# Kernel optimization log

Hardware: AMD Instinct MI355X
Metric: run time of the kernel (lower is better)

The kernel has to match this reference:

```python
import jax, jax.numpy as jnp
import numpy as np

DIM = 1024
HEADS = 16
DIM_HEAD = DIM // HEADS
SCALE = DIM_HEAD ** -0.5


def setup_inputs() -> dict:
    key = jax.random.key(0)
    k1, k2, k3 = jax.random.split(key, 3)
    x = jax.random.normal(k1, (4, 2048, DIM), dtype=jnp.float32)
    # q_lin: Linear(dim, 3*dim, bias=False); store as [dim, 3*dim] for x @ W
    w_qkv = jax.random.normal(k2, (DIM, 3 * DIM), dtype=jnp.float32) * (DIM ** -0.5)
    w_out = jax.random.normal(k3, (DIM, DIM), dtype=jnp.float32) * (DIM ** -0.5)
    return {"x": x, "w_qkv": w_qkv, "w_out": w_out}


def reference(x, w_qkv, w_out):
    b, n, d = x.shape
    qkv = x @ w_qkv  # [b, n, 3d]
    q, k, v = jnp.split(qkv, 3, axis=-1)
    # b n (h d) -> b h n d
    def to_heads(t):
        return t.reshape(b, n, HEADS, DIM_HEAD).transpose(0, 2, 1, 3)
    q, k, v = to_heads(q), to_heads(k), to_heads(v)
    sim = jnp.einsum('bhnj,bhmj->bhnm', q, k) * SCALE
    causal = jnp.triu(jnp.ones((n, n), dtype=bool), k=1)
    sim = jnp.where(causal, -jnp.finfo(sim.dtype).max, sim)
    attn = jax.nn.softmax(sim, axis=-1)
    out = jnp.einsum('bhnm,bhmd->bhnd', attn, v)
    out = out.transpose(0, 2, 1, 3).reshape(b, n, d)  # b h n d -> b n (h d)
    return out @ w_out
```

## Files before the change

kernel.cpp:

```cpp
#include <hip/hip_runtime.h>
#include <hip/hip_bf16.h>
#include <stdint.h>

#define SEQ  2048
#define DIMM 1024
#define NH   16
#define DH   64
#define NB   4
#define MROWS (NB*SEQ)
#define QKP  2080

typedef __attribute__((ext_vector_type(8))) short bf16x8;
typedef __attribute__((ext_vector_type(4))) float f32x4;
typedef __attribute__((ext_vector_type(16))) float f32x16;

#define LOG2E 1.44269504088896340736f

__device__ __forceinline__ unsigned short f2bf(float f) {
    union { float f; uint32_t u; } c; c.f = f;
    uint32_t r = c.u + 0x7fff + ((c.u >> 16) & 1);
    return (unsigned short)(r >> 16);
}

__device__ __forceinline__ void gload_lds16(const void* g, void* lds) {
    __builtin_amdgcn_global_load_lds(
        (const __attribute__((address_space(1))) unsigned int*)(g),
        (__attribute__((address_space(3))) unsigned int*)(lds),
        16, 0, 0);
}

__global__ __launch_bounds__(256) void k_prep(const float* __restrict__ x,
                                              unsigned short* __restrict__ x_bf,
                                              const float* __restrict__ w_qkv,
                                              unsigned short* __restrict__ wqkvT,
                                              const float* __restrict__ w_out,
                                              unsigned short* __restrict__ woutT) {
    __shared__ unsigned short tile[32][33];
    const int bid = blockIdx.x;
    if (bid < 8192) {
        int i = bid * 256 + threadIdx.x;
        float4 v = ((const float4*)x)[i];
        ushort4 o;
        o.x = f2bf(v.x); o.y = f2bf(v.y); o.z = f2bf(v.z); o.w = f2bf(v.w);
        ((ushort4*)x_bf)[i] = o;
        return;
    }
    const float* W;
    unsigned short* Wt;
    int tn, tk, N;
    if (bid < 8192 + 3072) {
        W = w_qkv; Wt = wqkvT; N = 3072;
        tn = (bid - 8192) % 96; tk = (bid - 8192) / 96;
    } else {
        W = w_out; Wt = woutT; N = 1024;
        tn = (bid - 11264) % 32; tk = (bid - 11264) / 32;
    }
    const int K = 1024;
    int lx = threadIdx.x & 31, ly = threadIdx.x >> 5;
    #pragma unroll
    for (int i = 0; i < 32; i += 8) {
        int k = tk * 32 + ly + i;
        int n = tn * 32 + lx;
        tile[ly + i][lx] = f2bf(W[(size_t)k * N + n]);
    }
    __syncthreads();
    int k2 = tk * 32 + lx;
    #pragma unroll
    for (int i = 0; i < 32; i += 8) {
        int n2 = tn * 32 + ly + i;
        Wt[(size_t)n2 * K + k2] = tile[lx][ly + i];
    }
}

template<int MODE>
__global__ __launch_bounds__(256) void k_gemm_bt(const unsigned short* __restrict__ A,
                                                 const unsigned short* __restrict__ Bt,
                                                 void* __restrict__ Cv,
                                                 unsigned short* __restrict__ vtv,
                                                 int M, int N_, int K) {
    constexpr int BM = 128, BN = 128, BK = 64;
    __shared__ unsigned short lA[BM * BK];
    __shared__ unsigned short lB[BN * BK];
    const int ntile = N_ / BN;
    const int tm = blockIdx.x / ntile;
    const int tn = blockIdx.x % ntile;
    const int t = threadIdx.x;
    const int w = t >> 6, l = t & 63;
    const int wr = w >> 1, wc = w & 1;

    const unsigned short* Abase = A + (size_t)tm * BM * K;
    const unsigned short* Bbase = Bt + (size_t)tn * BN * K;

    f32x4 acc[4][4] = {};

    const int rswz = (l & 7) << 4;

    for (int k0 = 0; k0 < K; k0 += BK) {
        __syncthreads();
        #pragma unroll
        for (int i = 0; i < 4; ++i) {
            const int o  = i * 4096 + t * 16;
            const int so = o ^ (((o >> 7) & 7) << 4);
            const int row = so >> 7;
            const int kb  = so & 127;
            gload_lds16((const char*)(Abase + (size_t)row * K + k0) + kb,
                        (char*)lA + i * 4096 + w * 1024);
            gload_lds16((const char*)(Bbase + (size_t)row * K + k0) + kb,
                        (char*)lB + i * 4096 + w * 1024);
        }
        __syncthreads();

        #pragma unroll
        for (int kk = 0; kk < 2; ++kk) {
            bf16x8 af[4], bfv[4];
            #pragma unroll
            for (int i = 0; i < 4; ++i) {
                const int ea = ((wr * 64 + i * 16 + (l & 15)) << 7) + kk * 64 + ((l >> 4) << 4);
                af[i] = *(const bf16x8*)((const char*)lA + (ea ^ rswz));
            }
            #pragma unroll
            for (int j = 0; j < 4; ++j) {
                const int eb = ((wc * 64 + j * 16 + (l & 15)) << 7) + kk * 64 + ((l >> 4) << 4);
                bfv[j] = *(const bf16x8*)((const char*)lB + (eb ^ rswz));
            }
            #pragma unroll
            for (int i = 0; i < 4; ++i)
                #pragma unroll
                for (int j = 0; j < 4; ++j)
                    acc[i][j] = __builtin_amdgcn_mfma_f32_16x16x32_bf16(af[i], bfv[j], acc[i][j], 0, 0, 0);
        }
    }

    const int row0 = tm * BM + wr * 64 + (l >> 4) * 4;
    const int col0 = tn * BN + wc * 64 + (l & 15);

    if (MODE == 0) {
        float* Cf = (float*)Cv;
        #pragma unroll
        for (int i = 0; i < 4; ++i)
            #pragma unroll
            for (int j = 0; j < 4; ++j)
                #pragma unroll
                for (int r = 0; r < 4; ++r)
                    Cf[(size_t)(row0 + i * 16 + r) * N_ + (col0 + j * 16)] = acc[i][j][r];
    } else if (tn < 16) {
        const float cs = (tn < 8) ? 0.125f * LOG2E : 1.0f;
        unsigned short* qk = (unsigned short*)Cv;
        #pragma unroll
        for (int i = 0; i < 4; ++i)
            #pragma unroll
            for (int j = 0; j < 4; ++j)
                #pragma unroll
                for (int r = 0; r < 4; ++r)
                    qk[(size_t)(row0 + i * 16 + r) * QKP + (col0 + j * 16)] = f2bf(acc[i][j][r] * cs);
    } else {
        #pragma unroll
        for (int i = 0; i < 4; ++i) {
            const int rbase = row0 + i * 16;
            const int bq = rbase >> 11;
            const int n0 = rbase & 2047;
            #pragma unroll
            for (int j = 0; j < 4; ++j) {
                const int c = col0 + j * 16 - 2048;
                const int hh = c >> 6, dd = c & 63;
                uint2 u;
                u.x = (unsigned int)f2bf(acc[i][j][0]) | ((unsigned int)f2bf(acc[i][j][1]) << 16);
                u.y = (unsigned int)f2bf(acc[i][j][2]) | ((unsigned int)f2bf(acc[i][j][3]) << 16);
                *(uint2*)(vtv + ((size_t)(bq * 16 + hh) * 64 + dd) * QKP + n0) = u;
            }
        }
    }
}

__global__ __launch_bounds__(256, 2) void k_attn16(const unsigned short* __restrict__ qk,
                                                   const unsigned short* __restrict__ vt,
                                                   unsigned short* __restrict__ out) {
    const int wid = (blockIdx.x & 7) * 64 + (blockIdx.x >> 3);
    const int bh = wid >> 3;
    const int pair = wid & 7;
    const int b = bh >> 4, h = bh & 15;
    const int w = threadIdx.x >> 6, l = threadIdx.x & 63;
    const int l31 = l & 31, hi = l >> 5;

    const unsigned short* qp = qk + (size_t)(b * SEQ) * QKP + h * 64;
    unsigned short* op = out + (size_t)(b * SEQ) * DIMM + h * 64;

    constexpr int KSTEP = 64 * QKP * 2;
    constexpr int VSTEP = 64 * 2;

    union U8 { uint32_t u[4]; bf16x8 v; };

    for (int ci = 0; ci < 2; ++ci) {
        const int chunk = ci ? pair : 15 - pair;
        const int q0w = chunk * 128 + w * 32;
        const int qrow = q0w + l31;
        const int nt = (q0w >> 6) + 1;

        bf16x8 qf[4];
        #pragma unroll
        for (int m = 0; m < 4; ++m)
            qf[m] = *(const bf16x8*)(qp + (size_t)(q0w + l31) * QKP + m * 16 + hi * 8);

        f32x16 accO0 = {}, accO1 = {};
        float m_run = -INFINITY, l_run = 0.f;

        const char* kp0 = (const char*)(qk + ((size_t)b * SEQ + l31) * QKP + 1024 + h * 64 + hi * 8);
        const char* kp1 = kp0 + 32 * QKP * 2;
        const char* vp0 = (const char*)(vt + ((size_t)bh * 64 + l31) * QKP + hi * 8);
        const char* vp1 = vp0 + 32 * QKP * 2;

        bf16x8 kf[2][4];
        #pragma unroll
        for (int m = 0; m < 4; ++m) {
            kf[0][m] = *(const bf16x8*)(kp0 + m * 32);
            kf[1][m] = *(const bf16x8*)(kp1 + m * 32);
        }
        kp0 += KSTEP; kp1 += KSTEP;

        for (int kt = 0; kt < nt; ++kt) {
            const int kv0 = kt * 64;
            const bool msk = (kt == nt - 1);

            f32x16 s0 = {}, s1 = {};
            __builtin_amdgcn_s_setprio(1);
            #pragma unroll
            for (int m = 0; m < 4; ++m) {
                s0 = __builtin_amdgcn_mfma_f32_32x32x16_bf16(kf[0][m], qf[m], s0, 0, 0, 0);
                s1 = __builtin_amdgcn_mfma_f32_32x32x16_bf16(kf[1][m], qf[m], s1, 0, 0, 0);
            }
            __builtin_amdgcn_s_setprio(0);

            bf16x8 vf0[4], vf1[4];
            #pragma unroll
            for (int m = 0; m < 4; ++m) {
                vf0[m] = *(const bf16x8*)(vp0 + m * 32);
                vf1[m] = *(const bf16x8*)(vp1 + m * 32);
            }
            vp0 += VSTEP; vp1 += VSTEP;

            #pragma unroll
            for (int m = 0; m < 4; ++m) {
                kf[0][m] = *(const bf16x8*)(kp0 + m * 32);
                kf[1][m] = *(const bf16x8*)(kp1 + m * 32);
            }
            kp0 += KSTEP; kp1 += KSTEP;

            float tmax = -1e30f;
            #pragma unroll
            for (int r = 0; r < 16; ++r) {
                const int crow = (r & 3) + 8 * (r >> 2) + 4 * hi;
                float v0 = s0[r];
                float v1 = s1[r];
                if (msk) {
                    if (kv0 + crow > qrow)      v0 = -1e30f;
                    if (kv0 + 32 + crow > qrow) v1 = -1e30f;
                }
                s0[r] = v0; s1[r] = v1;
                tmax = fmaxf(tmax, fmaxf(v0, v1));
            }
            tmax = fmaxf(tmax, __shfl_xor(tmax, 32));
            const bool defer = __all(tmax <= m_run + 8.0f);
            float fct = 1.0f;
            if (!defer) {
                const float mnew = fmaxf(m_run, tmax);
                fct = exp2f(m_run - mnew);
                m_run = mnew;
                #pragma unroll
                for (int r = 0; r < 16; ++r) { accO0[r] *= fct; accO1[r] *= fct; }
            }
            float ps = 0.f;
            #pragma unroll
            for (int r = 0; r < 16; ++r) {
                float p0 = exp2f(s0[r] - m_run);
                float p1 = exp2f(s1[r] - m_run);
                s0[r] = p0; s1[r] = p1;
                ps += p0 + p1;
            }
            ps += __shfl_xor(ps, 32);
            l_run = l_run * fct + ps;

            uint32_t pw0[8], pw1[8];
            #pragma unroll
            for (int i = 0; i < 8; ++i) {
                asm("v_cvt_pk_bf16_f32 %0, %1, %2" : "=v"(pw0[i]) : "v"(s0[2*i]), "v"(s0[2*i+1]));
                asm("v_cvt_pk_bf16_f32 %0, %1, %2" : "=v"(pw1[i]) : "v"(s1[2*i]), "v"(s1[2*i+1]));
            }
            __builtin_amdgcn_s_setprio(1);
            #define PVCHUNK(PW, BASE, VF0, VF1) do {                                     \
                uint32_t a0 = PW[BASE+0], b0 = PW[BASE+2];                               \
                uint32_t a1 = PW[BASE+1], b1 = PW[BASE+3];                               \
                asm("v_permlane32_swap_b32 %0, %1" : "+v"(a0), "+v"(b0));                \
                asm("v_permlane32_swap_b32 %0, %1" : "+v"(a1), "+v"(b1));                \
                U8 pb; pb.u[0] = a0; pb.u[1] = a1; pb.u[2] = b0; pb.u[3] = b1;           \
                accO0 = __builtin_amdgcn_mfma_f32_32x32x16_bf16(VF0, pb.v, accO0, 0, 0, 0); \
                accO1 = __builtin_amdgcn_mfma_f32_32x32x16_bf16(VF1, pb.v, accO1, 0, 0, 0); \
            } while (0)
            PVCHUNK(pw0, 0, vf0[0], vf1[0]);
            PVCHUNK(pw0, 4, vf0[1], vf1[1]);
            PVCHUNK(pw1, 0, vf0[2], vf1[2]);
            PVCHUNK(pw1, 4, vf0[3], vf1[3]);
            #undef PVCHUNK
            __builtin_amdgcn_s_setprio(0);
        }

        const float inv = 1.0f / l_run;
        unsigned short* orow = op + (size_t)(q0w + l31) * DIMM;
        #pragma unroll
        for (int g = 0; g < 4; ++g) {
            uint2 u0, u1;
            float a0 = accO0[4*g+0] * inv, a1 = accO0[4*g+1] * inv;
            float a2 = accO0[4*g+2] * inv, a3 = accO0[4*g+3] * inv;
            float c0 = accO1[4*g+0] * inv, c1 = accO1[4*g+1] * inv;
            float c2 = accO1[4*g+2] * inv, c3 = accO1[4*g+3] * inv;
            asm("v_cvt_pk_bf16_f32 %0, %1, %2" : "=v"(u0.x) : "v"(a0), "v"(a1));
            asm("v_cvt_pk_bf16_f32 %0, %1, %2" : "=v"(u0.y) : "v"(a2), "v"(a3));
            asm("v_cvt_pk_bf16_f32 %0, %1, %2" : "=v"(u1.x) : "v"(c0), "v"(c1));
            asm("v_cvt_pk_bf16_f32 %0, %1, %2" : "=v"(u1.y) : "v"(c2), "v"(c3));
            *(uint2*)(orow + 8*g + 4*hi)      = u0;
            *(uint2*)(orow + 32 + 8*g + 4*hi) = u1;
        }
    }
}

extern "C" void kernel_launch(void* const* d_in, const int* in_sizes, int n_in,
                              void* d_out, int out_size, void* d_ws, size_t ws_size,
                              hipStream_t stream) {
    const float* x     = (const float*)d_in[0];
    const float* w_qkv = (const float*)d_in[1];
    const float* w_out = (const float*)d_in[2];

    unsigned short* x_bf   = (unsigned short*)d_ws;
    unsigned short* wqkvT  = x_bf   + (size_t)MROWS * DIMM;
    unsigned short* woutT  = wqkvT  + (size_t)3 * DIMM * DIMM;
    unsigned short* qk_buf = woutT  + (size_t)DIMM * DIMM;
    unsigned short* vt     = qk_buf + (size_t)MROWS * QKP;
    unsigned short* aout   = vt     + (size_t)64 * DH * QKP;

    k_prep<<<8192 + 3072 + 1024, 256, 0, stream>>>(x, x_bf, w_qkv, wqkvT, w_out, woutT);

    k_gemm_bt<1><<<(MROWS / 128) * (3 * DIMM / 128), 256, 0, stream>>>(
        x_bf, wqkvT, qk_buf, vt, MROWS, 3 * DIMM, DIMM);

    k_attn16<<<NB * NH * 8, 256, 0, stream>>>(qk_buf, vt, aout);

    k_gemm_bt<0><<<(MROWS / 128) * (DIMM / 128), 256, 0, stream>>>(
        aout, woutT, d_out, nullptr, MROWS, DIMM, DIMM);
}
```

Baseline: 199.4 us.

## Share K/V tiles across waves via double-buffered LDS and remap GEMM workgroups

The attention kernel now stages each 64-row K and V tile into a double-buffered, swizzled LDS buffer using async global-to-LDS loads. All four waves of a block share that tile instead of each wave reading K/V from global memory on its own, and a block barrier runs every iteration. The GEMM kernels also remap the workgroup index so consecutive tiles are strided across the eight chiplets (XCDs), which is meant to improve L2 locality. The cost is extra LDS use and synchronisation, plus idle waves during the causal tail iterations, since the block loop runs to the longest wave's count.

```diff
diff --git a/kernel.cpp b/kernel.cpp
--- a/kernel.cpp
+++ b/kernel.cpp
@@ -82,8 +82,9 @@
     __shared__ unsigned short lA[BM * BK];
     __shared__ unsigned short lB[BN * BK];
     const int ntile = N_ / BN;
-    const int tm = blockIdx.x / ntile;
-    const int tn = blockIdx.x % ntile;
+    const int wgid = (blockIdx.x & 7) * (gridDim.x >> 3) + (blockIdx.x >> 3);
+    const int tm = wgid / ntile;
+    const int tn = wgid % ntile;
     const int t = threadIdx.x;
     const int w = t >> 6, l = t & 63;
     const int wr = w >> 1, wc = w & 1;
@@ -92,7 +93,6 @@
     const unsigned short* Bbase = Bt + (size_t)tn * BN * K;
 
     f32x4 acc[4][4] = {};
-
     const int rswz = (l & 7) << 4;
 
     for (int k0 = 0; k0 < K; k0 += BK) {
@@ -101,11 +101,9 @@
         for (int i = 0; i < 4; ++i) {
             const int o  = i * 4096 + t * 16;
             const int so = o ^ (((o >> 7) & 7) << 4);
-            const int row = so >> 7;
-            const int kb  = so & 127;
-            gload_lds16((const char*)(Abase + (size_t)row * K + k0) + kb,
+            gload_lds16((const char*)(Abase + (size_t)(so >> 7) * K + k0) + (so & 127),
                         (char*)lA + i * 4096 + w * 1024);
-            gload_lds16((const char*)(Bbase + (size_t)row * K + k0) + kb,
+            gload_lds16((const char*)(Bbase + (size_t)(so >> 7) * K + k0) + (so & 127),
                         (char*)lB + i * 4096 + w * 1024);
         }
         __syncthreads();
@@ -172,29 +170,47 @@
     }
 }
 
-__global__ __launch_bounds__(256, 2) void k_attn16(const unsigned short* __restrict__ qk,
+__global__ __launch_bounds__(256, 2) void k_attn22(const unsigned short* __restrict__ qk,
                                                    const unsigned short* __restrict__ vt,
                                                    unsigned short* __restrict__ out) {
     const int wid = (blockIdx.x & 7) * 64 + (blockIdx.x >> 3);
     const int bh = wid >> 3;
     const int pair = wid & 7;
     const int b = bh >> 4, h = bh & 15;
-    const int w = threadIdx.x >> 6, l = threadIdx.x & 63;
+    const int t = threadIdx.x;
+    const int w = t >> 6, l = t & 63;
     const int l31 = l & 31, hi = l >> 5;
+
+    __shared__ unsigned short Kl[2][64 * 64];
+    __shared__ unsigned short Vl[2][64 * 64];
 
     const unsigned short* qp = qk + (size_t)(b * SEQ) * QKP + h * 64;
     unsigned short* op = out + (size_t)(b * SEQ) * DIMM + h * 64;
-
-    constexpr int KSTEP = 64 * QKP * 2;
-    constexpr int VSTEP = 64 * 2;
-
+    const char* kbase = (const char*)(qk + (size_t)(b * SEQ) * QKP + 1024 + h * 64);
+    const char* vbase = (const char*)(vt + (size_t)bh * 64 * QKP);
+
+    const int rswz = (l & 7) << 4;
     union U8 { uint32_t u[4]; bf16x8 v; };
 
+    auto STAGE = [&](int kv0, int bs) {
+        #pragma unroll
+        for (int i = 0; i < 2; ++i) {
+            const int o  = i * 4096 + t * 16;
+            const int so = o ^ (((o >> 7) & 7) << 4);
+            const int row = so >> 7, cb = so & 127;
+            gload_lds16(kbase + (size_t)(kv0 + row) * (QKP * 2) + cb,
+                        (char*)Kl[bs] + i * 4096 + w * 1024);
+            gload_lds16(vbase + (size_t)row * (QKP * 2) + kv0 * 2 + cb,
+                        (char*)Vl[bs] + i * 4096 + w * 1024);
+        }
+    };
+
     for (int ci = 0; ci < 2; ++ci) {
-        const int chunk = ci ? pair : 15 - pair;
-        const int q0w = chunk * 128 + w * 32;
+        const int c = ci ? pair : 15 - pair;
+        const int q0w = c * 128 + w * 32;
         const int qrow = q0w + l31;
-        const int nt = (q0w >> 6) + 1;
+        const int ntw = (q0w >> 6) + 1;
+        const int ntb = c * 2 + 2;
 
         bf16x8 qf[4];
         #pragma unroll
@@ -204,103 +220,104 @@
         f32x16 accO0 = {}, accO1 = {};
         float m_run = -INFINITY, l_run = 0.f;
 
-        const char* kp0 = (const char*)(qk + ((size_t)b * SEQ + l31) * QKP + 1024 + h * 64 + hi * 8);
-        const char* kp1 = kp0 + 32 * QKP * 2;
-        const char* vp0 = (const char*)(vt + ((size_t)bh * 64 + l31) * QKP + hi * 8);
-        const char* vp1 = vp0 + 32 * QKP * 2;
-
-        bf16x8 kf[2][4];
-        #pragma unroll
-        for (int m = 0; m < 4; ++m) {
-            kf[0][m] = *(const bf16x8*)(kp0 + m * 32);
-            kf[1][m] = *(const bf16x8*)(kp1 + m * 32);
-        }
-        kp0 += KSTEP; kp1 += KSTEP;
-
-        for (int kt = 0; kt < nt; ++kt) {
-            const int kv0 = kt * 64;
-            const bool msk = (kt == nt - 1);
-
-            f32x16 s0 = {}, s1 = {};
-            __builtin_amdgcn_s_setprio(1);
-            #pragma unroll
-            for (int m = 0; m < 4; ++m) {
-                s0 = __builtin_amdgcn_mfma_f32_32x32x16_bf16(kf[0][m], qf[m], s0, 0, 0, 0);
-                s1 = __builtin_amdgcn_mfma_f32_32x32x16_bf16(kf[1][m], qf[m], s1, 0, 0, 0);
+        STAGE(0, 0);
+        __syncthreads();
+
+        for (int kt = 0; kt < ntb; ++kt) {
+            if (kt + 1 < ntb) STAGE((kt + 1) * 64, (kt + 1) & 1);
+
+            if (kt < ntw) {
+                const int kv0 = kt * 64;
+                const bool msk = (kt == ntw - 1);
+                const char* kl = (const char*)Kl[kt & 1];
+                const char* vl = (const char*)Vl[kt & 1];
+
+                bf16x8 kf[2][4];
+                #pragma unroll
+                for (int f = 0; f < 2; ++f)
+                    #pragma unroll
+                    for (int m = 0; m < 4; ++m) {
+                        const int ea = ((f * 32 + l31) << 7) + m * 32 + hi * 16;
+                        kf[f][m] = *(const bf16x8*)(kl + (ea ^ rswz));
+                    }
+
+                f32x16 s0 = {}, s1 = {};
+                __builtin_amdgcn_s_setprio(1);
+                #pragma unroll
+                for (int m = 0; m < 4; ++m) {
+                    s0 = __builtin_amdgcn_mfma_f32_32x32x16_bf16(kf[0][m], qf[m], s0, 0, 0, 0);
+                    s1 = __builtin_amdgcn_mfma_f32_32x32x16_bf16(kf[1][m], qf[m], s1, 0, 0, 0);
+                }
+                __builtin_amdgcn_s_setprio(0);
+
+                bf16x8 vf0[4], vf1[4];
+                #pragma unroll
+                for (int m = 0; m < 4; ++m) {
+                    const int e0 = (l31 << 7) + m * 32 + hi * 16;
+                    const int e1 = ((32 + l31) << 7) + m * 32 + hi * 16;
+                    vf0[m] = *(const bf16x8*)(vl + (e0 ^ rswz));
+                    vf1[m] = *(const bf16x8*)(vl + (e1 ^ rswz));
+                }
+
+                float tmax = -1e30f;
+                #pragma unroll
+                for (int r = 0; r < 16; ++r) {
+                    float v0 = s0[r];
+                    float v1 = s1[r];
+                    if (msk) {
+                        const int crow = (r & 3) + 8 * (r >> 2) + 4 * hi;
+                        if (kv0 + crow > qrow)      v0 = -1e30f;
+                        if (kv0 + 32 + crow > qrow) v1 = -1e30f;
+                        s0[r] = v0; s1[r] = v1;
+                    }
+                    tmax = fmaxf(tmax, fmaxf(v0, v1));
+                }
+                tmax = fmaxf(tmax, __shfl_xor(tmax, 32));
+                const bool defer = __all(tmax <= m_run + 8.0f);
+                float fct = 1.0f;
+                if (!defer) {
+                    const float mnew = fmaxf(m_run, tmax);
+                    fct = exp2f(m_run - mnew);
+                    m_run = mnew;
+                    #pragma unroll
+                    for (int r = 0; r < 16; ++r) { accO0[r] *= fct; accO1[r] *= fct; }
+                }
+                float ps = 0.f;
+                #pragma unroll
+                for (int r = 0; r < 16; ++r) {
+                    float p0 = exp2f(s0[r] - m_run);
+                    float p1 = exp2f(s1[r] - m_run);
+                    s0[r] = p0; s1[r] = p1;
+                    ps += p0 + p1;
+                }
+                ps += __shfl_xor(ps, 32);
+                l_run = l_run * fct + ps;
+
+                uint32_t pw0[8], pw1[8];
+                #pragma unroll
+                for (int i = 0; i < 8; ++i) {
+                    asm("v_cvt_pk_bf16_f32 %0, %1, %2" : "=v"(pw0[i]) : "v"(s0[2*i]), "v"(s0[2*i+1]));
+                    asm("v_cvt_pk_bf16_f32 %0, %1, %2" : "=v"(pw1[i]) : "v"(s1[2*i]), "v"(s1[2*i+1]));
+                }
+                __builtin_amdgcn_s_setprio(1);
+                #define PVCHUNK(PW, BASE, VF0, VF1) do {                                     \
+                    uint32_t a0 = PW[BASE+0], b0 = PW[BASE+2];                               \
+                    uint32_t a1 = PW[BASE+1], b1 = PW[BASE+3];                               \
+                    asm("v_permlane32_swap_b32 %0, %1" : "+v"(a0), "+v"(b0));                \
+                    asm("v_permlane32_swap_b32 %0, %1" : "+v"(a1), "+v"(b1));                \
+                    U8 pb; pb.u[0] = a0; pb.u[1] = a1; pb.u[2] = b0; pb.u[3] = b1;           \
+                    accO0 = __builtin_amdgcn_mfma_f32_32x32x16_bf16(VF0, pb.v, accO0, 0, 0, 0); \
+                    accO1 = __builtin_amdgcn_mfma_f32_32x32x16_bf16(VF1, pb.v, accO1, 0, 0, 0); \
+                } while (0)
+                PVCHUNK(pw0, 0, vf0[0], vf1[0]);
+                PVCHUNK(pw0, 4, vf0[1], vf1[1]);
+                PVCHUNK(pw1, 0, vf0[2], vf1[2]);
+                PVCHUNK(pw1, 4, vf0[3], vf1[3]);
+                #undef PVCHUNK
+                __builtin_amdgcn_s_setprio(0);
             }
-            __builtin_amdgcn_s_setprio(0);
-
-            bf16x8 vf0[4], vf1[4];
-            #pragma unroll
-            for (int m = 0; m < 4; ++m) {
-                vf0[m] = *(const bf16x8*)(vp0 + m * 32);
-                vf1[m] = *(const bf16x8*)(vp1 + m * 32);
-            }
-            vp0 += VSTEP; vp1 += VSTEP;
-
-            #pragma unroll
-            for (int m = 0; m < 4; ++m) {
-                kf[0][m] = *(const bf16x8*)(kp0 + m * 32);
-                kf[1][m] = *(const bf16x8*)(kp1 + m * 32);
-            }
-            kp0 += KSTEP; kp1 += KSTEP;
-
-            float tmax = -1e30f;
-            #pragma unroll
-            for (int r = 0; r < 16; ++r) {
-                const int crow = (r & 3) + 8 * (r >> 2) + 4 * hi;
-                float v0 = s0[r];
-                float v1 = s1[r];
-                if (msk) {
-                    if (kv0 + crow > qrow)      v0 = -1e30f;
-                    if (kv0 + 32 + crow > qrow) v1 = -1e30f;
-                }
-                s0[r] = v0; s1[r] = v1;
-                tmax = fmaxf(tmax, fmaxf(v0, v1));
-            }
-            tmax = fmaxf(tmax, __shfl_xor(tmax, 32));
-            const bool defer = __all(tmax <= m_run + 8.0f);
-            float fct = 1.0f;
-            if (!defer) {
-                const float mnew = fmaxf(m_run, tmax);
-                fct = exp2f(m_run - mnew);
-                m_run = mnew;
-                #pragma unroll
-                for (int r = 0; r < 16; ++r) { accO0[r] *= fct; accO1[r] *= fct; }
-            }
-            float ps = 0.f;
-            #pragma unroll
-            for (int r = 0; r < 16; ++r) {
-                float p0 = exp2f(s0[r] - m_run);
-                float p1 = exp2f(s1[r] - m_run);
-                s0[r] = p0; s1[r] = p1;
-                ps += p0 + p1;
-            }
-            ps += __shfl_xor(ps, 32);
-            l_run = l_run * fct + ps;
-
-            uint32_t pw0[8], pw1[8];
-            #pragma unroll
-            for (int i = 0; i < 8; ++i) {
-                asm("v_cvt_pk_bf16_f32 %0, %1, %2" : "=v"(pw0[i]) : "v"(s0[2*i]), "v"(s0[2*i+1]));
-                asm("v_cvt_pk_bf16_f32 %0, %1, %2" : "=v"(pw1[i]) : "v"(s1[2*i]), "v"(s1[2*i+1]));
-            }
-            __builtin_amdgcn_s_setprio(1);
-            #define PVCHUNK(PW, BASE, VF0, VF1) do {                                     \
-                uint32_t a0 = PW[BASE+0], b0 = PW[BASE+2];                               \
-                uint32_t a1 = PW[BASE+1], b1 = PW[BASE+3];                               \
-                asm("v_permlane32_swap_b32 %0, %1" : "+v"(a0), "+v"(b0));                \
-                asm("v_permlane32_swap_b32 %0, %1" : "+v"(a1), "+v"(b1));                \
-                U8 pb; pb.u[0] = a0; pb.u[1] = a1; pb.u[2] = b0; pb.u[3] = b1;           \
-                accO0 = __builtin_amdgcn_mfma_f32_32x32x16_bf16(VF0, pb.v, accO0, 0, 0, 0); \
-                accO1 = __builtin_amdgcn_mfma_f32_32x32x16_bf16(VF1, pb.v, accO1, 0, 0, 0); \
-            } while (0)
-            PVCHUNK(pw0, 0, vf0[0], vf1[0]);
-            PVCHUNK(pw0, 4, vf0[1], vf1[1]);
-            PVCHUNK(pw1, 0, vf0[2], vf1[2]);
-            PVCHUNK(pw1, 4, vf0[3], vf1[3]);
-            #undef PVCHUNK
-            __builtin_amdgcn_s_setprio(0);
+
+            __syncthreads();
         }
 
         const float inv = 1.0f / l_run;
@@ -341,7 +358,7 @@
     k_gemm_bt<1><<<(MROWS / 128) * (3 * DIMM / 128), 256, 0, stream>>>(
         x_bf, wqkvT, qk_buf, vt, MROWS, 3 * DIMM, DIMM);
 
-    k_attn16<<<NB * NH * 8, 256, 0, stream>>>(qk_buf, vt, aout);
+    k_attn22<<<NB * NH * 8, 256, 0, stream>>>(qk_buf, vt, aout);
 
     k_gemm_bt<0><<<(MROWS / 128) * (DIMM / 128), 256, 0, stream>>>(
         aout, woutT, d_out, nullptr, MROWS, DIMM, DIMM);
```

New measurement: 182.9 us. 8.3% less time.
